# Kernel tuning notes

Hardware: AMD Instinct MI355X
Metric: run time of the kernel (lower is better)

The kernel has to match this reference:

```python
import jax, jax.numpy as jnp
import numpy as np

TEMP_UPDATE = 1e-05
EPS = 1e-12  # torch F.normalize eps


def _l2norm(x, axis):
    n = jnp.sqrt(jnp.sum(x * x, axis=axis, keepdims=True))
    return x / jnp.maximum(n, EPS)


def setup_inputs() -> dict:
    key = jax.random.key(0)
    k1, k2 = jax.random.split(key)
    query = jax.random.normal(k1, (64, 256, 512), dtype=jnp.float32)
    keys = jax.random.normal(k2, (2048, 512), dtype=jnp.float32)
    return {"query": query, "keys": keys}


def reference(query, keys):
    bs, t, d = query.shape
    m = keys.shape[0]
    # F.normalize(query, dim=2)
    q = _l2norm(query, axis=2)
    qr = q.reshape(bs * t, d)                      # [N, d]
    score = qr @ keys.T                            # [N, m]
    score_query = jax.nn.softmax(score, axis=0)    # softmax over queries per slot
    score_memory = jax.nn.softmax(score, axis=1)   # softmax over slots per query
    # topk(1) over memory dim -> argmax slot per query
    g = jnp.argmax(score_memory, axis=1)           # [N] int
    col_max = jnp.max(score_query, axis=0)         # [m]
    # weight per query: score_query[n, g_n] / max(score_query[:, g_n])
    w = jnp.take_along_axis(score_query, g[:, None], axis=1)[:, 0] / col_max[g]
    # fused scatter-add replacing the per-slot python loop
    query_update = jax.ops.segment_sum(w[:, None] * qr, g, num_segments=m)  # [m, d]
    updated = _l2norm(TEMP_UPDATE * query_update + keys, axis=1)
    return jax.lax.stop_gradient(updated)  # original returns .detach()
```

## Files before the change

kernel.cpp:

```cpp
#include <hip/hip_runtime.h>
#include <math.h>

#define N_Q     16384
#define DDIM    512
#define M_SLOTS 2048
#define EPSN    1e-12f
#define TEMPU   1e-5f
#define KSCALE  25.4f
#define QSCALE  127.0f
#define INV_S   (1.0f / (127.0f * 25.4f))

typedef unsigned int u32;
typedef unsigned long long u64;
typedef __attribute__((ext_vector_type(4))) int i32x4;

__device__ __forceinline__ void gld_lds16(const void* g, void* l) {
    __builtin_amdgcn_global_load_lds(
        (const __attribute__((address_space(1))) u32*)(g),
        (__attribute__((address_space(3))) u32*)(l), 16, 0, 0);
}
__device__ __forceinline__ float block_reduce_sum_128(float v, float* sred, int t) {
    #pragma unroll
    for (int o = 32; o > 0; o >>= 1) v += __shfl_down(v, o, 64);
    if ((t & 63) == 0) sred[t >> 6] = v;
    __syncthreads();
    return sred[0] + sred[1];
}
__device__ __forceinline__ char q8(float x, float s) {
    int v = __float2int_rn(x * s);
    v = v < -127 ? -127 : (v > 127 ? 127 : v);
    return (char)v;
}

__global__ __launch_bounds__(128) void k_prep(const float* __restrict__ q,
                                              const float* __restrict__ keys,
                                              char* __restrict__ qi8,
                                              char* __restrict__ ki8) {
    __shared__ float sred[2];
    int b = blockIdx.x;
    int t = threadIdx.x;
    if (b < N_Q) {
        float4 v = ((const float4*)(q + (size_t)b * DDIM))[t];
        float ss = v.x * v.x + v.y * v.y + v.z * v.z + v.w * v.w;
        ss = block_reduce_sum_128(ss, sred, t);
        float s = QSCALE / fmaxf(sqrtf(ss), EPSN);
        char4 o;
        o.x = q8(v.x, s);
        o.y = q8(v.y, s);
        o.z = q8(v.z, s);
        o.w = q8(v.w, s);
        ((char4*)(qi8 + (size_t)b * DDIM))[t] = o;
    } else {
        int r = b - N_Q;
        float4 v = ((const float4*)(keys + (size_t)r * DDIM))[t];
        char4 o;
        o.x = q8(v.x, KSCALE);
        o.y = q8(v.y, KSCALE);
        o.z = q8(v.z, KSCALE);
        o.w = q8(v.w, KSCALE);
        ((char4*)(ki8 + (size_t)r * DDIM))[t] = o;
    }
}

__global__ __launch_bounds__(256) void k_score(const char* __restrict__ qi8,
                                               const char* __restrict__ ki8,
                                               u64* __restrict__ rowpack,
                                               int* __restrict__ colmax) {
    __shared__ char sA[2][128 * 64];
    __shared__ char sB[2][128 * 64];

    int t = threadIdx.x;
    int lane = t & 63;
    int wid = t >> 6;
    int wrow = wid >> 1;
    int wcol = wid & 1;
    int lr = lane & 15;
    int kc = lane >> 4;

    int n0 = blockIdx.y * 128;
    int j0 = blockIdx.x * 128;

    int srow = t >> 2;
    int scolB = (t & 3) * 16;

    const char* gA0 = qi8 + (size_t)(n0 + srow) * DDIM + scolB;
    const char* gA1 = qi8 + (size_t)(n0 + 64 + srow) * DDIM + scolB;
    const char* gB0 = ki8 + (size_t)(j0 + srow) * DDIM + scolB;
    const char* gB1 = ki8 + (size_t)(j0 + 64 + srow) * DDIM + scolB;

    i32x4 acc[4][4] = {};

#define STAGE(buf, k0)  do {                                   \
        gld_lds16(gA0 + (k0), &sA[buf][t * 16]);               \
        gld_lds16(gA1 + (k0), &sA[buf][4096 + t * 16]);        \
        gld_lds16(gB0 + (k0), &sB[buf][t * 16]);               \
        gld_lds16(gB1 + (k0), &sB[buf][4096 + t * 16]);        \
    } while (0)

    STAGE(0, 0);
    __syncthreads();

    #pragma unroll
    for (int kt = 0; kt < 8; ++kt) {
        const int cur = kt & 1;
        if (kt < 7) STAGE(cur ^ 1, (kt + 1) * 64);

        i32x4 a[4], b[4];
        #pragma unroll
        for (int i = 0; i < 4; ++i)
            a[i] = *(const i32x4*)&sA[cur][(wrow * 64 + i * 16 + lr) * 64 + kc * 16];
        #pragma unroll
        for (int j = 0; j < 4; ++j)
            b[j] = *(const i32x4*)&sB[cur][(wcol * 64 + j * 16 + lr) * 64 + kc * 16];
        #pragma unroll
        for (int i = 0; i < 4; ++i)
            #pragma unroll
            for (int j = 0; j < 4; ++j)
                acc[i][j] = __builtin_amdgcn_mfma_i32_16x16x64_i8(a[i], b[j], acc[i][j], 0, 0, 0);

        if (kt < 7) __syncthreads();
    }
#undef STAGE

    #pragma unroll
    for (int i = 0; i < 4; ++i) {
        #pragma unroll
        for (int r = 0; r < 4; ++r) {
            int v = acc[i][0][r];
            int c = j0 + wcol * 64 + lr;
            #pragma unroll
            for (int j = 1; j < 4; ++j) {
                int vj = acc[i][j][r];
                int cj = j0 + wcol * 64 + j * 16 + lr;
                if (vj > v) { v = vj; c = cj; }
            }
            #pragma unroll
            for (int off = 1; off < 16; off <<= 1) {
                int ov = __shfl_xor(v, off, 64);
                int oc = __shfl_xor(c, off, 64);
                if (ov > v || (ov == v && oc < c)) { v = ov; c = oc; }
            }
            if (lr == 0) {
                int grow = n0 + wrow * 64 + i * 16 + kc * 4 + r;
                u64 pk = ((u64)(u32)(v ^ 0x80000000) << 32) | (u64)(~(u32)c);
                atomicMax(rowpack + grow, pk);
            }
        }
    }
    #pragma unroll
    for (int j = 0; j < 4; ++j) {
        int m = acc[0][j][0];
        #pragma unroll
        for (int i = 0; i < 4; ++i)
            #pragma unroll
            for (int r = 0; r < 4; ++r) m = max(m, acc[i][j][r]);
        m = max(m, __shfl_xor(m, 16, 64));
        m = max(m, __shfl_xor(m, 32, 64));
        if (kc == 0) atomicMax(colmax + j0 + wcol * 64 + j * 16 + lr, m);
    }
}

__global__ __launch_bounds__(256) void k_hist(const u64* __restrict__ rowpack,
                                              u32* __restrict__ cnt) {
    int n = blockIdx.x * 256 + threadIdx.x;
    u64 p = rowpack[n];
    int g = (int)(~(u32)(p & 0xFFFFFFFFull));
    atomicAdd(cnt + g, 1u);
}

__global__ __launch_bounds__(256) void k_scan(const u32* __restrict__ cnt,
                                              u32* __restrict__ start,
                                              u32* __restrict__ cursor) {
    __shared__ u32 wsum[4];
    int t = threadIdx.x;
    int lane = t & 63, w = t >> 6;
    u32 local[8], s = 0;
    #pragma unroll
    for (int i = 0; i < 8; ++i) { local[i] = cnt[t * 8 + i]; s += local[i]; }
    u32 x = s;
    #pragma unroll
    for (int off = 1; off < 64; off <<= 1) {
        u32 y = __shfl_up(x, off, 64);
        if (lane >= off) x += y;
    }
    if (lane == 63) wsum[w] = x;
    __syncthreads();
    u32 base = 0;
    #pragma unroll
    for (int i = 0; i < 4; ++i) if (i < w) base += wsum[i];
    u32 run = base + x - s;
    #pragma unroll
    for (int i = 0; i < 8; ++i) {
        start[t * 8 + i] = run;
        cursor[t * 8 + i] = run;
        run += local[i];
    }
}

__global__ __launch_bounds__(256) void k_fill(const u64* __restrict__ rowpack,
                                              const int* __restrict__ colmax,
                                              u32* __restrict__ cursor,
                                              u32* __restrict__ perm,
                                              float* __restrict__ wval) {
    int n = blockIdx.x * 256 + threadIdx.x;
    u64 p = rowpack[n];
    int vi = (int)(((u32)(p >> 32)) ^ 0x80000000u);
    int g = (int)(~(u32)(p & 0xFFFFFFFFull));
    int cm = colmax[g];
    float w = expf((float)(vi - cm) * INV_S);
    u32 pos = atomicAdd(cursor + g, 1u);
    perm[pos] = (u32)n;
    wval[pos] = w;
}

__global__ __launch_bounds__(128) void k_gather_final(const char* __restrict__ qi8,
                                                      const u32* __restrict__ start,
                                                      const u32* __restrict__ cnt,
                                                      const u32* __restrict__ perm,
                                                      const float* __restrict__ wval,
                                                      const float* __restrict__ keys,
                                                      float* __restrict__ out) {
    __shared__ float sred[2];
    int j = blockIdx.x;
    int t = threadIdx.x;
    u32 s = start[j];
    u32 e = s + cnt[j];
    float ax = 0.f, ay = 0.f, az = 0.f, aw = 0.f;
    for (u32 i = s; i < e; ++i) {
        u32 n = perm[i];
        float wq = wval[i] * (1.0f / 127.0f);
        char4 q4 = ((const char4*)(qi8 + (size_t)n * DDIM))[t];
        ax = fmaf(wq, (float)q4.x, ax);
        ay = fmaf(wq, (float)q4.y, ay);
        az = fmaf(wq, (float)q4.z, az);
        aw = fmaf(wq, (float)q4.w, aw);
    }
    float4 k4 = ((const float4*)(keys + (size_t)j * DDIM))[t];
    float4 v;
    v.x = fmaf(TEMPU, ax, k4.x);
    v.y = fmaf(TEMPU, ay, k4.y);
    v.z = fmaf(TEMPU, az, k4.z);
    v.w = fmaf(TEMPU, aw, k4.w);
    float ss = v.x * v.x + v.y * v.y + v.z * v.z + v.w * v.w;
    ss = block_reduce_sum_128(ss, sred, t);
    float inv = 1.0f / fmaxf(sqrtf(ss), EPSN);
    v.x *= inv; v.y *= inv; v.z *= inv; v.w *= inv;
    ((float4*)(out + (size_t)j * DDIM))[t] = v;
}

extern "C" void kernel_launch(void* const* d_in, const int* in_sizes, int n_in,
                              void* d_out, int out_size, void* d_ws, size_t ws_size,
                              hipStream_t stream) {
    const float* query = (const float*)d_in[0];
    const float* keys  = (const float*)d_in[1];
    float* out = (float*)d_out;

    char* ws = (char*)d_ws;
    const size_t OFF_QI8   = 0;
    const size_t OFF_ROW   = 8388608;
    const size_t OFF_CNT   = OFF_ROW + 131072;
    const size_t OFF_CMAX  = OFF_CNT + 8192;
    const size_t OFF_START = OFF_CMAX + 8192;
    const size_t OFF_CUR   = OFF_START + 8192;
    const size_t OFF_PERM  = OFF_CUR + 8192;
    const size_t OFF_W     = OFF_PERM + 65536;
    const size_t OFF_KI8   = OFF_W + 65536;

    char*   qi8    = ws + OFF_QI8;
    u64*    rowpack= (u64*)(ws + OFF_ROW);
    u32*    cnt    = (u32*)(ws + OFF_CNT);
    int*    cmax   = (int*)(ws + OFF_CMAX);
    u32*    start  = (u32*)(ws + OFF_START);
    u32*    cursor = (u32*)(ws + OFF_CUR);
    u32*    perm   = (u32*)(ws + OFF_PERM);
    float*  wval   = (float*)(ws + OFF_W);
    char*   ki8    = ws + OFF_KI8;

    hipMemsetAsync(ws + OFF_ROW, 0, 131072 + 8192, stream);
    hipMemsetAsync(ws + OFF_CMAX, 0x80, 8192, stream);

    k_prep<<<N_Q + M_SLOTS, 128, 0, stream>>>(query, keys, qi8, ki8);

    dim3 g2(M_SLOTS / 128, N_Q / 128);
    k_score<<<g2, 256, 0, stream>>>(qi8, ki8, rowpack, cmax);

    k_hist<<<N_Q / 256, 256, 0, stream>>>(rowpack, cnt);
    k_scan<<<1, 256, 0, stream>>>(cnt, start, cursor);
    k_fill<<<N_Q / 256, 256, 0, stream>>>(rowpack, cmax, cursor, perm, wval);
    k_gather_final<<<M_SLOTS, 128, 0, stream>>>(qi8, start, cnt, perm, wval, keys, out);
}
```

Before: 86.97 us.

## Triple-buffer int8 score GEMM with swizzled LDS and fold memsets into prep

```diff
diff --git a/kernel.cpp b/kernel.cpp
--- a/kernel.cpp
+++ b/kernel.cpp
@@ -9,6 +9,7 @@
 #define KSCALE  25.4f
 #define QSCALE  127.0f
 #define INV_S   (1.0f / (127.0f * 25.4f))
+#define NZBLK   72
 
 typedef unsigned int u32;
 typedef unsigned long long u64;
@@ -35,7 +36,8 @@
 __global__ __launch_bounds__(128) void k_prep(const float* __restrict__ q,
                                               const float* __restrict__ keys,
                                               char* __restrict__ qi8,
-                                              char* __restrict__ ki8) {
+                                              char* __restrict__ ki8,
+                                              float4* __restrict__ zbase) {
     __shared__ float sred[2];
     int b = blockIdx.x;
     int t = threadIdx.x;
@@ -50,7 +52,7 @@
         o.z = q8(v.z, s);
         o.w = q8(v.w, s);
         ((char4*)(qi8 + (size_t)b * DDIM))[t] = o;
-    } else {
+    } else if (b < N_Q + M_SLOTS) {
         int r = b - N_Q;
         float4 v = ((const float4*)(keys + (size_t)r * DDIM))[t];
         char4 o;
@@ -59,15 +61,18 @@
         o.z = q8(v.z, KSCALE);
         o.w = q8(v.w, KSCALE);
         ((char4*)(ki8 + (size_t)r * DDIM))[t] = o;
+    } else {
+        int idx = (b - (N_Q + M_SLOTS)) * 128 + t;
+        zbase[idx] = make_float4(0.f, 0.f, 0.f, 0.f);
     }
 }
 
 __global__ __launch_bounds__(256) void k_score(const char* __restrict__ qi8,
                                                const char* __restrict__ ki8,
                                                u64* __restrict__ rowpack,
-                                               int* __restrict__ colmax) {
-    __shared__ char sA[2][128 * 64];
-    __shared__ char sB[2][128 * 64];
+                                               u32* __restrict__ colmax) {
+    __shared__ char sA[3][128 * 64];
+    __shared__ char sB[3][128 * 64];
 
     int t = threadIdx.x;
     int lane = t & 63;
@@ -81,12 +86,15 @@
     int j0 = blockIdx.x * 128;
 
     int srow = t >> 2;
-    int scolB = (t & 3) * 16;
+    int scolB = 16 * ((t & 3) ^ ((t >> 3) & 3));
 
     const char* gA0 = qi8 + (size_t)(n0 + srow) * DDIM + scolB;
     const char* gA1 = qi8 + (size_t)(n0 + 64 + srow) * DDIM + scolB;
     const char* gB0 = ki8 + (size_t)(j0 + srow) * DDIM + scolB;
     const char* gB1 = ki8 + (size_t)(j0 + 64 + srow) * DDIM + scolB;
+
+    int rsw = 16 * ((t >> 1) & 3);
+    (void)rsw;
 
     i32x4 acc[4][4] = {};
 
@@ -98,27 +106,41 @@
     } while (0)
 
     STAGE(0, 0);
-    __syncthreads();
+    STAGE(1, 64);
+    asm volatile("s_waitcnt vmcnt(4)" ::: "memory");
+    __builtin_amdgcn_s_barrier();
+    __builtin_amdgcn_sched_barrier(0);
+
+    const int rchunk = 16 * 0;
+    (void)rchunk;
 
     #pragma unroll
     for (int kt = 0; kt < 8; ++kt) {
-        const int cur = kt & 1;
-        if (kt < 7) STAGE(cur ^ 1, (kt + 1) * 64);
+        const int cur = kt % 3;
+        if (kt < 6) STAGE((kt + 2) % 3, (kt + 2) * 64);
 
         i32x4 a[4], b[4];
+        int roff = 16 * (kc ^ ((lr >> 1) & 3));
         #pragma unroll
         for (int i = 0; i < 4; ++i)
-            a[i] = *(const i32x4*)&sA[cur][(wrow * 64 + i * 16 + lr) * 64 + kc * 16];
+            a[i] = *(const i32x4*)&sA[cur][(wrow * 64 + i * 16 + lr) * 64 + roff];
         #pragma unroll
         for (int j = 0; j < 4; ++j)
-            b[j] = *(const i32x4*)&sB[cur][(wcol * 64 + j * 16 + lr) * 64 + kc * 16];
+            b[j] = *(const i32x4*)&sB[cur][(wcol * 64 + j * 16 + lr) * 64 + roff];
+        __builtin_amdgcn_s_setprio(1);
         #pragma unroll
         for (int i = 0; i < 4; ++i)
             #pragma unroll
             for (int j = 0; j < 4; ++j)
                 acc[i][j] = __builtin_amdgcn_mfma_i32_16x16x64_i8(a[i], b[j], acc[i][j], 0, 0, 0);
-
-        if (kt < 7) __syncthreads();
+        __builtin_amdgcn_s_setprio(0);
+
+        if (kt < 6)       asm volatile("s_waitcnt vmcnt(4)" ::: "memory");
+        else if (kt == 6) asm volatile("s_waitcnt vmcnt(0)" ::: "memory");
+        if (kt < 7) {
+            __builtin_amdgcn_s_barrier();
+            __builtin_amdgcn_sched_barrier(0);
+        }
     }
 #undef STAGE
 
@@ -156,7 +178,8 @@
             for (int r = 0; r < 4; ++r) m = max(m, acc[i][j][r]);
         m = max(m, __shfl_xor(m, 16, 64));
         m = max(m, __shfl_xor(m, 32, 64));
-        if (kc == 0) atomicMax(colmax + j0 + wcol * 64 + j * 16 + lr, m);
+        if (kc == 0) atomicMax(colmax + j0 + wcol * 64 + j * 16 + lr,
+                               (u32)m ^ 0x80000000u);
     }
 }
 
@@ -198,7 +221,7 @@
 }
 
 __global__ __launch_bounds__(256) void k_fill(const u64* __restrict__ rowpack,
-                                              const int* __restrict__ colmax,
+                                              const u32* __restrict__ colmax,
                                               u32* __restrict__ cursor,
                                               u32* __restrict__ perm,
                                               float* __restrict__ wval) {
@@ -206,7 +229,7 @@
     u64 p = rowpack[n];
     int vi = (int)(((u32)(p >> 32)) ^ 0x80000000u);
     int g = (int)(~(u32)(p & 0xFFFFFFFFull));
-    int cm = colmax[g];
+    int cm = (int)(colmax[g] ^ 0x80000000u);
     float w = expf((float)(vi - cm) * INV_S);
     u32 pos = atomicAdd(cursor + g, 1u);
     perm[pos] = (u32)n;
@@ -258,9 +281,9 @@
     char* ws = (char*)d_ws;
     const size_t OFF_QI8   = 0;
     const size_t OFF_ROW   = 8388608;
-    const size_t OFF_CNT   = OFF_ROW + 131072;
-    const size_t OFF_CMAX  = OFF_CNT + 8192;
-    const size_t OFF_START = OFF_CMAX + 8192;
+    const size_t OFF_CMAX  = OFF_ROW + 131072;
+    const size_t OFF_CNT   = OFF_CMAX + 8192;
+    const size_t OFF_START = OFF_CNT + 8192;
     const size_t OFF_CUR   = OFF_START + 8192;
     const size_t OFF_PERM  = OFF_CUR + 8192;
     const size_t OFF_W     = OFF_PERM + 65536;
@@ -268,18 +291,16 @@
 
     char*   qi8    = ws + OFF_QI8;
     u64*    rowpack= (u64*)(ws + OFF_ROW);
+    u32*    cmax   = (u32*)(ws + OFF_CMAX);
     u32*    cnt    = (u32*)(ws + OFF_CNT);
-    int*    cmax   = (int*)(ws + OFF_CMAX);
     u32*    start  = (u32*)(ws + OFF_START);
     u32*    cursor = (u32*)(ws + OFF_CUR);
     u32*    perm   = (u32*)(ws + OFF_PERM);
     float*  wval   = (float*)(ws + OFF_W);
     char*   ki8    = ws + OFF_KI8;
 
-    hipMemsetAsync(ws + OFF_ROW, 0, 131072 + 8192, stream);
-    hipMemsetAsync(ws + OFF_CMAX, 0x80, 8192, stream);
-
-    k_prep<<<N_Q + M_SLOTS, 128, 0, stream>>>(query, keys, qi8, ki8);
+    k_prep<<<N_Q + M_SLOTS + NZBLK, 128, 0, stream>>>(query, keys, qi8, ki8,
+                                                      (float4*)(ws + OFF_ROW));
 
     dim3 g2(M_SLOTS / 128, N_Q / 128);
     k_score<<<g2, 256, 0, stream>>>(qi8, ki8, rowpack, cmax);
```

After: 84.88 us. 2.4% less time.
